# Optimization experiments

Measured on AMD Instinct MI355X. Metric: run time of the kernel, lower is better.

## Reference

```python
import jax, jax.numpy as jnp
import numpy as np
from jax.scipy.special import logsumexp

SINKHORN_ITERS = 10


def _fix_coupling_sinkhorn(lc, lp1, lp2, iterations=SINKHORN_ITERS):
    # lc: [Z,S], lp1: [Z], lp2: [S]
    for _ in range(iterations):
        lc = lc + lp1[:, None] - logsumexp(lc, axis=1, keepdims=True)
        lc = lc + lp2[None, :] - logsumexp(lc, axis=0, keepdims=True)
    return lc


def _fix_coupling_rejection(lc, lp1, lp2):
    fixed_p1 = lc + lp1[:, None] - logsumexp(lc, axis=1, keepdims=True)
    approx_lp2 = logsumexp(fixed_p1, axis=0)
    accept = lp2 - approx_lp2
    accept = accept - jnp.max(accept)
    acc_s2_given_s1 = jax.nn.log_softmax(fixed_p1, axis=-1) + accept[None, :]
    log_keep = logsumexp(acc_s2_given_s1, axis=-1)
    certainly_keep = jnp.exp(log_keep) >= 1.0
    resample = jnp.where(
        certainly_keep, -jnp.inf,
        jnp.log1p(-jnp.where(certainly_keep, 0.0, jnp.exp(log_keep))))
    compensation = resample[:, None] + lp2[None, :]
    return lp1[:, None] + jnp.logaddexp(acc_s2_given_s1, compensation)


def setup_inputs() -> dict:
    key = jax.random.key(0)
    ks = jax.random.split(key, 8)
    B, S, Z, H1, H2 = 64, 512, 1024, 512, 256
    return {
        "s_logits": jax.random.normal(ks[0], (B, S), jnp.float32),
        "W1": jax.random.normal(ks[1], (S, H1), jnp.float32) / np.sqrt(S),
        "b1": jnp.zeros((H1,), jnp.float32),
        "W2": jax.random.normal(ks[2], (H1, H2), jnp.float32) / np.sqrt(H1),
        "b2": jnp.zeros((H2,), jnp.float32),
        "Wout": jax.random.normal(ks[3], (H2, Z, S), jnp.float32) / np.sqrt(H2),
        "bout": jnp.zeros((Z, S), jnp.float32),
        "prior": jax.random.normal(ks[4], (Z,), jnp.float32) * 0.05,
    }


def reference(s_logits, W1, b1, W2, b2, Wout, bout, prior):
    z_logits = jax.nn.log_softmax(prior)  # [Z]

    def get_joint(sl):  # sl: [S]
        v = jax.nn.softmax(sl)
        v = jax.nn.sigmoid(v @ W1 + b1)
        v = jax.nn.sigmoid(v @ W2 + b2)
        log_joint = jnp.einsum('h,hzs->zs', v, Wout) + bout  # [Z,S]
        log_joint = _fix_coupling_sinkhorn(log_joint, z_logits, sl)
        return _fix_coupling_rejection(log_joint, z_logits, sl)

    return jax.vmap(get_joint)(s_logits)  # [B,Z,S]
```

## Files before the change

kernel.cpp:

```cpp
#include <hip/hip_runtime.h>
#include <math.h>

#define Bn 64
#define Sn 512
#define Zn 1024
#define H1n 512
#define H2n 256
#define ZSn (Zn*Sn)

#define OFF_LP1  0
#define OFF_VML  1024
#define OFF_U    17408
#define OFF_V    82944
#define OFF_R    115712
#define OFF_W    181248
#define OFF_RES  214016
#define OFF_PM   279552
#define OFF_PS   541696

__device__ __forceinline__ float wred_max(float x){
#pragma unroll
  for (int o=32;o;o>>=1) x = fmaxf(x, __shfl_xor(x, o, 64));
  return x;
}
__device__ __forceinline__ float wred_sum(float x){
#pragma unroll
  for (int o=32;o;o>>=1) x += __shfl_xor(x, o, 64);
  return x;
}
__device__ __forceinline__ float lae(float a, float c){
  float m = fmaxf(a,c), n = fminf(a,c);
  return m + log1pf(__expf(n-m));
}

__global__ __launch_bounds__(512) void prep_kernel(const float* __restrict__ prior,
                                                   float* __restrict__ ws){
  int b = blockIdx.x, t = threadIdx.x;
  if (b < Bn){ ws[OFF_V + b*Sn + t] = 0.f; return; }
  __shared__ float red[8];
  float x0 = prior[t], x1 = prior[t+512];
  float m = wred_max(fmaxf(x0,x1));
  if ((t&63)==0) red[t>>6] = m;
  __syncthreads();
  float M = red[0];
#pragma unroll
  for (int i=1;i<8;i++) M = fmaxf(M, red[i]);
  float e = __expf(x0-M)+__expf(x1-M);
  e = wred_sum(e);
  __syncthreads();
  if ((t&63)==0) red[t>>6] = e;
  __syncthreads();
  float T = 0.f;
#pragma unroll
  for (int i=0;i<8;i++) T += red[i];
  float lse = M + logf(T);
  ws[OFF_LP1 + t]       = x0 - lse;
  ws[OFF_LP1 + t + 512] = x1 - lse;
}

__global__ __launch_bounds__(512) void mlp_kernel(const float* __restrict__ sl,
    const float* __restrict__ W1, const float* __restrict__ b1,
    const float* __restrict__ W2, const float* __restrict__ b2,
    float* __restrict__ ws){
  __shared__ float p[Sn];
  __shared__ float h1s[H1n];
  __shared__ float red[8];
  int b = blockIdx.x, t = threadIdx.x;
  float x = sl[b*Sn + t];
  float m = wred_max(x);
  if ((t&63)==0) red[t>>6] = m;
  __syncthreads();
  float M = red[0];
#pragma unroll
  for (int i=1;i<8;i++) M = fmaxf(M, red[i]);
  float e = __expf(x-M);
  float es = wred_sum(e);
  __syncthreads();
  if ((t&63)==0) red[t>>6] = es;
  __syncthreads();
  float T = 0.f;
#pragma unroll
  for (int i=0;i<8;i++) T += red[i];
  p[t] = e / T;
  __syncthreads();
  float acc = b1[t];
#pragma unroll 8
  for (int s=0;s<Sn;s++) acc = fmaf(p[s], W1[s*H1n + t], acc);
  h1s[t] = 1.f/(1.f+__expf(-acc));
  __syncthreads();
  if (t < H2n){
    float a2 = b2[t];
#pragma unroll 8
    for (int s=0;s<H1n;s++) a2 = fmaf(h1s[s], W2[s*H2n + t], a2);
    ws[OFF_VML + b*H2n + t] = 1.f/(1.f+__expf(-a2));
  }
}

__global__ __launch_bounds__(256,2) void gemm_kernel(const float* __restrict__ Wout,
    const float* __restrict__ bout, const float* __restrict__ ws, float* __restrict__ K){
  int zh = blockIdx.x*256 + threadIdx.x;
  const float* V = ws + OFF_VML;
  float2 acc[Bn];
#pragma unroll
  for (int b=0;b<Bn;b++){ acc[b].x = 0.f; acc[b].y = 0.f; }
  const float2* Wp = (const float2*)Wout;
  for (int h=0; h<H2n; h++){
    float2 wv = Wp[(size_t)h*(ZSn/2) + zh];
#pragma unroll
    for (int b=0;b<Bn;b++){
      float vb = V[b*H2n + h];
      acc[b].x = fmaf(vb, wv.x, acc[b].x);
      acc[b].y = fmaf(vb, wv.y, acc[b].y);
    }
  }
  float2 bb = ((const float2*)bout)[zh];
#pragma unroll
  for (int b=0;b<Bn;b++){
    float2 o; o.x = acc[b].x + bb.x; o.y = acc[b].y + bb.y;
    ((float2*)(K + (size_t)b*ZSn))[zh] = o;
  }
}

__global__ __launch_bounds__(256) void row_pass(const float* __restrict__ K,
    float* __restrict__ ws, int vecoff, int mode){
  int row = blockIdx.x*4 + (threadIdx.x>>6);
  int l = threadIdx.x & 63;
  int b = row >> 10, z = row & (Zn-1);
  const float4* Kr = (const float4*)(K + (size_t)row*Sn);
  const float4* Vr = (const float4*)(ws + vecoff + b*Sn);
  float4 k0 = Kr[l], k1 = Kr[l+64];
  float4 v0 = Vr[l], v1 = Vr[l+64];
  float x0=k0.x+v0.x, x1=k0.y+v0.y, x2=k0.z+v0.z, x3=k0.w+v0.w;
  float x4=k1.x+v1.x, x5=k1.y+v1.y, x6=k1.z+v1.z, x7=k1.w+v1.w;
  float m = fmaxf(fmaxf(fmaxf(x0,x1),fmaxf(x2,x3)), fmaxf(fmaxf(x4,x5),fmaxf(x6,x7)));
  m = wred_max(m);
  float s = __expf(x0-m)+__expf(x1-m)+__expf(x2-m)+__expf(x3-m)
          + __expf(x4-m)+__expf(x5-m)+__expf(x6-m)+__expf(x7-m);
  s = wred_sum(s);
  if (l==0){
    float L = m + logf(s);
    if (mode==0){
      ws[OFF_U + row] = ws[OFF_LP1 + z] - L;
    } else if (mode==1){
      ws[OFF_R + row] = L;
      ws[OFF_U + row] = ws[OFF_LP1 + z] - L;
    } else {
      float lk = L - ws[OFF_R + row];
      ws[OFF_RES + row] = (lk >= 0.f) ? -__builtin_inff() : log1pf(-__expf(lk));
    }
  }
}

__global__ __launch_bounds__(512) void col_pass1(const float* __restrict__ K,
                                                 float* __restrict__ ws){
  int bzc = blockIdx.x; int b = bzc >> 3, zc = bzc & 7, s = threadIdx.x;
  const float* Kb = K + (size_t)b*ZSn + (size_t)zc*128*Sn;
  const float* ub = ws + OFF_U + b*Zn + zc*128;
  float m = -__builtin_inff(), sum = 0.f;
#pragma unroll 4
  for (int i=0;i<128;i++){
    float x = Kb[i*Sn + s] + ub[i];
    float nm = fmaxf(m, x);
    sum = sum*__expf(m-nm) + __expf(x-nm);
    m = nm;
  }
  ws[OFF_PM + bzc*Sn + s] = m;
  ws[OFF_PS + bzc*Sn + s] = sum;
}

__global__ __launch_bounds__(512) void col_pass2(float* __restrict__ ws,
    const float* __restrict__ sl, int modeB){
  int b = blockIdx.x, s = threadIdx.x;
  float M = -__builtin_inff(), T = 0.f;
#pragma unroll
  for (int zc=0;zc<8;zc++){
    float m = ws[OFF_PM + (b*8+zc)*Sn + s];
    float t = ws[OFF_PS + (b*8+zc)*Sn + s];
    float nM = fmaxf(M, m);
    T = T*__expf(M-nM) + t*__expf(m-nM);
    M = nM;
  }
  float L = M + logf(T);
  float lp2 = sl[b*Sn + s];
  if (!modeB){
    ws[OFF_V + b*Sn + s] = lp2 - L;
  } else {
    __shared__ float red[8];
    float vv = ws[OFF_V + b*Sn + s];
    float araw = lp2 - vv - L;
    float mm = wred_max(araw);
    if ((s&63)==0) red[s>>6] = mm;
    __syncthreads();
    float amax = red[0];
#pragma unroll
    for (int i=1;i<8;i++) amax = fmaxf(amax, red[i]);
    ws[OFF_W + b*Sn + s] = vv + araw - amax;
  }
}

__global__ __launch_bounds__(256) void final_kernel(float* __restrict__ K,
    const float* __restrict__ ws, const float* __restrict__ sl){
  int idx4 = blockIdx.x*256 + threadIdx.x;
  int row = idx4 >> 7;
  int c4  = idx4 & 127;
  int b = row >> 10, z = row & (Zn-1);
  float r  = ws[OFF_R + row];
  float rs = ws[OFF_RES + row];
  float l1 = ws[OFF_LP1 + z];
  float4 k = ((const float4*)K)[idx4];
  float4 w = ((const float4*)(ws + OFF_W + b*Sn))[c4];
  float4 p = ((const float4*)(sl + (size_t)b*Sn))[c4];
  float4 o;
  o.x = l1 + lae(k.x - r + w.x, rs + p.x);
  o.y = l1 + lae(k.y - r + w.y, rs + p.y);
  o.z = l1 + lae(k.z - r + w.z, rs + p.z);
  o.w = l1 + lae(k.w - r + w.w, rs + p.w);
  ((float4*)K)[idx4] = o;
}

extern "C" void kernel_launch(void* const* d_in, const int* in_sizes, int n_in,
                              void* d_out, int out_size, void* d_ws, size_t ws_size,
                              hipStream_t stream) {
  const float* sl    = (const float*)d_in[0];
  const float* W1    = (const float*)d_in[1];
  const float* b1    = (const float*)d_in[2];
  const float* W2    = (const float*)d_in[3];
  const float* b2    = (const float*)d_in[4];
  const float* Wout  = (const float*)d_in[5];
  const float* bout  = (const float*)d_in[6];
  const float* prior = (const float*)d_in[7];
  float* K  = (float*)d_out;
  float* ws = (float*)d_ws;

  prep_kernel<<<Bn+1, 512, 0, stream>>>(prior, ws);
  mlp_kernel<<<Bn, 512, 0, stream>>>(sl, W1, b1, W2, b2, ws);
  gemm_kernel<<<ZSn/512, 256, 0, stream>>>(Wout, bout, ws, K);

  for (int it = 0; it < 10; ++it){
    row_pass <<<Bn*Zn/4, 256, 0, stream>>>(K, ws, OFF_V, 0);
    col_pass1<<<Bn*8,    512, 0, stream>>>(K, ws);
    col_pass2<<<Bn,      512, 0, stream>>>(ws, sl, 0);
  }
  row_pass <<<Bn*Zn/4, 256, 0, stream>>>(K, ws, OFF_V, 1);
  col_pass1<<<Bn*8,    512, 0, stream>>>(K, ws);
  col_pass2<<<Bn,      512, 0, stream>>>(ws, sl, 1);
  row_pass <<<Bn*Zn/4, 256, 0, stream>>>(K, ws, OFF_W, 2);

  final_kernel<<<(Bn*(size_t)ZSn/4)/256, 256, 0, stream>>>(K, ws, sl);
}
```

Baseline: 1.615 ms.

## Fuse Sinkhorn row/col passes, store logits in bf16, fuse final rejection

Replaces the per-iteration row_pass, col_pass1 and col_pass2 launches with one fused kernel. That kernel stages a 64-row tile of the logits in shared memory, does the row logsumexp, and emits column partials. The previous iteration's column reduction is folded into the next launch. When the workspace is large enough, the GEMM output is stored as bf16 in workspace, halving the traffic of every Sinkhorn sweep. The final rejection step is also fused into one row kernel, and the V matrix is transposed for the GEMM. The bf16 storage loses precision relative to the fp32 reference, and the fused kernel uses a large shared-memory tile that limits occupancy.

New measurement: 1.478 ms. -8.5%, faster.

```diff
diff --git a/kernel.cpp b/kernel.cpp
--- a/kernel.cpp
+++ b/kernel.cpp
@@ -9,14 +9,16 @@
 #define ZSn (Zn*Sn)
 
 #define OFF_LP1  0
-#define OFF_VML  1024
-#define OFF_U    17408
-#define OFF_V    82944
-#define OFF_R    115712
-#define OFF_W    181248
-#define OFF_RES  214016
-#define OFF_PM   279552
-#define OFF_PS   541696
+#define OFF_VT   1024
+#define OFF_V    17408
+#define OFF_W    50176
+#define OFF_R    82944
+#define OFF_PM   148480
+#define OFF_PS   672768
+#define OFF_KB   1310720
+#define NEED_BF16_BYTES ((size_t)OFF_KB*4 + (size_t)Bn*ZSn*2)
+
+#define NINF (-__builtin_inff())
 
 __device__ __forceinline__ float wred_max(float x){
 #pragma unroll
@@ -32,12 +34,19 @@
   float m = fmaxf(a,c), n = fminf(a,c);
   return m + log1pf(__expf(n-m));
 }
+__device__ __forceinline__ float toF(float v){ return v; }
+__device__ __forceinline__ float toF(unsigned short v){ return __uint_as_float(((unsigned int)v)<<16); }
+__device__ __forceinline__ unsigned int pack2(float a, float b){
+  unsigned int ua = __float_as_uint(a), ub = __float_as_uint(b);
+  ua = (ua + 0x7fffu + ((ua>>16)&1u)) >> 16;
+  ub = (ub + 0x7fffu + ((ub>>16)&1u)) & 0xffff0000u;
+  return ua | ub;
+}
 
 __global__ __launch_bounds__(512) void prep_kernel(const float* __restrict__ prior,
                                                    float* __restrict__ ws){
-  int b = blockIdx.x, t = threadIdx.x;
-  if (b < Bn){ ws[OFF_V + b*Sn + t] = 0.f; return; }
   __shared__ float red[8];
+  int t = threadIdx.x;
   float x0 = prior[t], x1 = prior[t+512];
   float m = wred_max(fmaxf(x0,x1));
   if ((t&63)==0) red[t>>6] = m;
@@ -92,130 +101,165 @@
     float a2 = b2[t];
 #pragma unroll 8
     for (int s=0;s<H1n;s++) a2 = fmaf(h1s[s], W2[s*H2n + t], a2);
-    ws[OFF_VML + b*H2n + t] = 1.f/(1.f+__expf(-a2));
-  }
-}
-
-__global__ __launch_bounds__(256,2) void gemm_kernel(const float* __restrict__ Wout,
-    const float* __restrict__ bout, const float* __restrict__ ws, float* __restrict__ K){
+    ws[OFF_VT + t*Bn + b] = 1.f/(1.f+__expf(-a2));
+  }
+}
+
+template<int BF>
+__global__ __launch_bounds__(256,1) void gemm_kernel(const float* __restrict__ Wout,
+    const float* __restrict__ bout, const float* __restrict__ ws,
+    float* __restrict__ Kf, unsigned int* __restrict__ Kb){
   int zh = blockIdx.x*256 + threadIdx.x;
-  const float* V = ws + OFF_VML;
+  const float* __restrict__ VT = ws + OFF_VT;
   float2 acc[Bn];
 #pragma unroll
   for (int b=0;b<Bn;b++){ acc[b].x = 0.f; acc[b].y = 0.f; }
   const float2* Wp = (const float2*)Wout;
+#pragma unroll 2
   for (int h=0; h<H2n; h++){
     float2 wv = Wp[(size_t)h*(ZSn/2) + zh];
+    const float* vh = VT + (h<<6);
 #pragma unroll
     for (int b=0;b<Bn;b++){
-      float vb = V[b*H2n + h];
-      acc[b].x = fmaf(vb, wv.x, acc[b].x);
-      acc[b].y = fmaf(vb, wv.y, acc[b].y);
+      acc[b].x = fmaf(vh[b], wv.x, acc[b].x);
+      acc[b].y = fmaf(vh[b], wv.y, acc[b].y);
     }
   }
   float2 bb = ((const float2*)bout)[zh];
 #pragma unroll
   for (int b=0;b<Bn;b++){
-    float2 o; o.x = acc[b].x + bb.x; o.y = acc[b].y + bb.y;
-    ((float2*)(K + (size_t)b*ZSn))[zh] = o;
-  }
-}
-
-__global__ __launch_bounds__(256) void row_pass(const float* __restrict__ K,
-    float* __restrict__ ws, int vecoff, int mode){
-  int row = blockIdx.x*4 + (threadIdx.x>>6);
-  int l = threadIdx.x & 63;
+    float ax = acc[b].x + bb.x, ay = acc[b].y + bb.y;
+    if (BF){
+      Kb[(size_t)b*(ZSn/2) + zh] = pack2(ax, ay);
+    } else {
+      float2 o; o.x = ax; o.y = ay;
+      ((float2*)Kf)[(size_t)b*(ZSn/2) + zh] = o;
+    }
+  }
+}
+
+template<typename KT>
+__global__ __launch_bounds__(512) void iter_fused(const KT* __restrict__ Kg,
+    float* __restrict__ ws, const float* __restrict__ sl, int iter, int mode){
+  __shared__ KT Ksh[64*512];
+  __shared__ float vsh[512];
+  __shared__ float ush[64];
+  __shared__ float lsh[64];
+  int t = threadIdx.x;
+  int b = blockIdx.x >> 4, c = blockIdx.x & 15;
+  const float4* s4 = (const float4*)(Kg + ((size_t)((b<<10) + (c<<6)) << 9));
+  float4* d4 = (float4*)Ksh;
+  constexpr int NV = (int)sizeof(KT)*4;
+#pragma unroll
+  for (int i=0;i<NV;i++) d4[i*512 + t] = s4[i*512 + t];
+  if (t < 64) lsh[t] = ws[OFF_LP1 + (c<<6) + t];
+  float v_s;
+  if (iter == 0) v_s = 0.f;
+  else {
+    float M = NINF, S = 0.f;
+#pragma unroll
+    for (int cc=0; cc<16; cc++){
+      float m = ws[OFF_PM + ((b*16+cc)<<9) + t];
+      float p = ws[OFF_PS + ((b*16+cc)<<9) + t];
+      float nm = fmaxf(M, m);
+      S = S*__expf(M-nm) + p*__expf(m-nm);
+      M = nm;
+    }
+    v_s = sl[(b<<9) + t] - (M + logf(S));
+  }
+  vsh[t] = v_s;
+  if (mode) ws[OFF_V + (b<<9) + t] = v_s;
+  __syncthreads();
+  int l = t & 63, w = t >> 6;
+#pragma unroll
+  for (int rr=0; rr<8; rr++){
+    int row = (w<<3) + rr;
+    float x[8];
+    float m = NINF;
+#pragma unroll
+    for (int j=0;j<8;j++){
+      x[j] = toF(Ksh[(row<<9) + (j<<6) + l]) + vsh[(j<<6)+l];
+      m = fmaxf(m, x[j]);
+    }
+    m = wred_max(m);
+    float s = 0.f;
+#pragma unroll
+    for (int j=0;j<8;j++) s += __expf(x[j]-m);
+    s = wred_sum(s);
+    float L = m + logf(s);
+    if (l == 0){
+      ush[row] = lsh[row] - L;
+      if (mode) ws[OFF_R + (b<<10) + (c<<6) + row] = L;
+    }
+  }
+  __syncthreads();
+  float M = NINF, S = 0.f;
+#pragma unroll 8
+  for (int i=0;i<64;i++){
+    float x2 = toF(Ksh[(i<<9) + t]) + ush[i];
+    float nm = fmaxf(M, x2);
+    S = S*__expf(M-nm) + __expf(x2-nm);
+    M = nm;
+  }
+  ws[OFF_PM + ((b*16+c)<<9) + t] = M;
+  ws[OFF_PS + ((b*16+c)<<9) + t] = S;
+}
+
+__global__ __launch_bounds__(512) void wker(float* __restrict__ ws, const float* __restrict__ sl){
+  __shared__ float red[8];
+  int b = blockIdx.x, s = threadIdx.x;
+  float M = NINF, S = 0.f;
+#pragma unroll
+  for (int cc=0; cc<16; cc++){
+    float m = ws[OFF_PM + ((b*16+cc)<<9) + s];
+    float p = ws[OFF_PS + ((b*16+cc)<<9) + s];
+    float nm = fmaxf(M, m);
+    S = S*__expf(M-nm) + p*__expf(m-nm);
+    M = nm;
+  }
+  float L = M + logf(S);
+  float v = ws[OFF_V + (b<<9) + s];
+  float araw = sl[(b<<9)+s] - v - L;
+  float mm = wred_max(araw);
+  if ((s&63)==0) red[s>>6] = mm;
+  __syncthreads();
+  float amax = red[0];
+#pragma unroll
+  for (int i=1;i<8;i++) amax = fmaxf(amax, red[i]);
+  ws[OFF_W + (b<<9) + s] = v + araw - amax;
+}
+
+template<typename KT>
+__global__ __launch_bounds__(512) void final_fused(const KT* Kg,
+    float* out, const float* __restrict__ ws, const float* __restrict__ sl){
+  int t = threadIdx.x, l = t & 63, wv = t >> 6;
+  int row = blockIdx.x*8 + wv;
   int b = row >> 10, z = row & (Zn-1);
-  const float4* Kr = (const float4*)(K + (size_t)row*Sn);
-  const float4* Vr = (const float4*)(ws + vecoff + b*Sn);
-  float4 k0 = Kr[l], k1 = Kr[l+64];
-  float4 v0 = Vr[l], v1 = Vr[l+64];
-  float x0=k0.x+v0.x, x1=k0.y+v0.y, x2=k0.z+v0.z, x3=k0.w+v0.w;
-  float x4=k1.x+v1.x, x5=k1.y+v1.y, x6=k1.z+v1.z, x7=k1.w+v1.w;
-  float m = fmaxf(fmaxf(fmaxf(x0,x1),fmaxf(x2,x3)), fmaxf(fmaxf(x4,x5),fmaxf(x6,x7)));
+  const KT* Kr = Kg + ((size_t)row << 9);
+  const float* wr = ws + OFF_W + (b << 9);
+  const float* pr = sl + (b << 9);
+  float r  = ws[OFF_R + row];
+  float l1 = ws[OFF_LP1 + z];
+  float k[8], a[8];
+  float m = NINF;
+#pragma unroll
+  for (int j=0;j<8;j++){
+    k[j] = toF(Kr[(j<<6)+l]);
+    a[j] = k[j] - r + wr[(j<<6)+l];
+    m = fmaxf(m, a[j]);
+  }
   m = wred_max(m);
-  float s = __expf(x0-m)+__expf(x1-m)+__expf(x2-m)+__expf(x3-m)
-          + __expf(x4-m)+__expf(x5-m)+__expf(x6-m)+__expf(x7-m);
+  float s = 0.f;
+#pragma unroll
+  for (int j=0;j<8;j++) s += __expf(a[j]-m);
   s = wred_sum(s);
-  if (l==0){
-    float L = m + logf(s);
-    if (mode==0){
-      ws[OFF_U + row] = ws[OFF_LP1 + z] - L;
-    } else if (mode==1){
-      ws[OFF_R + row] = L;
-      ws[OFF_U + row] = ws[OFF_LP1 + z] - L;
-    } else {
-      float lk = L - ws[OFF_R + row];
-      ws[OFF_RES + row] = (lk >= 0.f) ? -__builtin_inff() : log1pf(-__expf(lk));
-    }
-  }
-}
-
-__global__ __launch_bounds__(512) void col_pass1(const float* __restrict__ K,
-                                                 float* __restrict__ ws){
-  int bzc = blockIdx.x; int b = bzc >> 3, zc = bzc & 7, s = threadIdx.x;
-  const float* Kb = K + (size_t)b*ZSn + (size_t)zc*128*Sn;
-  const float* ub = ws + OFF_U + b*Zn + zc*128;
-  float m = -__builtin_inff(), sum = 0.f;
-#pragma unroll 4
-  for (int i=0;i<128;i++){
-    float x = Kb[i*Sn + s] + ub[i];
-    float nm = fmaxf(m, x);
-    sum = sum*__expf(m-nm) + __expf(x-nm);
-    m = nm;
-  }
-  ws[OFF_PM + bzc*Sn + s] = m;
-  ws[OFF_PS + bzc*Sn + s] = sum;
-}
-
-__global__ __launch_bounds__(512) void col_pass2(float* __restrict__ ws,
-    const float* __restrict__ sl, int modeB){
-  int b = blockIdx.x, s = threadIdx.x;
-  float M = -__builtin_inff(), T = 0.f;
-#pragma unroll
-  for (int zc=0;zc<8;zc++){
-    float m = ws[OFF_PM + (b*8+zc)*Sn + s];
-    float t = ws[OFF_PS + (b*8+zc)*Sn + s];
-    float nM = fmaxf(M, m);
-    T = T*__expf(M-nM) + t*__expf(m-nM);
-    M = nM;
-  }
-  float L = M + logf(T);
-  float lp2 = sl[b*Sn + s];
-  if (!modeB){
-    ws[OFF_V + b*Sn + s] = lp2 - L;
-  } else {
-    __shared__ float red[8];
-    float vv = ws[OFF_V + b*Sn + s];
-    float araw = lp2 - vv - L;
-    float mm = wred_max(araw);
-    if ((s&63)==0) red[s>>6] = mm;
-    __syncthreads();
-    float amax = red[0];
-#pragma unroll
-    for (int i=1;i<8;i++) amax = fmaxf(amax, red[i]);
-    ws[OFF_W + b*Sn + s] = vv + araw - amax;
-  }
-}
-
-__global__ __launch_bounds__(256) void final_kernel(float* __restrict__ K,
-    const float* __restrict__ ws, const float* __restrict__ sl){
-  int idx4 = blockIdx.x*256 + threadIdx.x;
-  int row = idx4 >> 7;
-  int c4  = idx4 & 127;
-  int b = row >> 10, z = row & (Zn-1);
-  float r  = ws[OFF_R + row];
-  float rs = ws[OFF_RES + row];
-  float l1 = ws[OFF_LP1 + z];
-  float4 k = ((const float4*)K)[idx4];
-  float4 w = ((const float4*)(ws + OFF_W + b*Sn))[c4];
-  float4 p = ((const float4*)(sl + (size_t)b*Sn))[c4];
-  float4 o;
-  o.x = l1 + lae(k.x - r + w.x, rs + p.x);
-  o.y = l1 + lae(k.y - r + w.y, rs + p.y);
-  o.z = l1 + lae(k.z - r + w.z, rs + p.z);
-  o.w = l1 + lae(k.w - r + w.w, rs + p.w);
-  ((float4*)K)[idx4] = o;
+  float lk = m + logf(s);
+  float rs = (lk >= 0.f) ? NINF : log1pf(-__expf(lk));
+  float* Or = out + ((size_t)row << 9);
+#pragma unroll
+  for (int j=0;j<8;j++){
+    Or[(j<<6)+l] = l1 + lae(a[j], rs + pr[(j<<6)+l]);
+  }
 }
 
 extern "C" void kernel_launch(void* const* d_in, const int* in_sizes, int n_in,
@@ -229,22 +273,27 @@
   const float* Wout  = (const float*)d_in[5];
   const float* bout  = (const float*)d_in[6];
   const float* prior = (const float*)d_in[7];
-  float* K  = (float*)d_out;
   float* ws = (float*)d_ws;
-
-  prep_kernel<<<Bn+1, 512, 0, stream>>>(prior, ws);
+  float* Kf = (float*)d_out;
+  unsigned short* Kb = (unsigned short*)(ws + OFF_KB);
+  const bool use_bf16 = (ws_size >= NEED_BF16_BYTES);
+
+  prep_kernel<<<1, 512, 0, stream>>>(prior, ws);
   mlp_kernel<<<Bn, 512, 0, stream>>>(sl, W1, b1, W2, b2, ws);
-  gemm_kernel<<<ZSn/512, 256, 0, stream>>>(Wout, bout, ws, K);
-
-  for (int it = 0; it < 10; ++it){
-    row_pass <<<Bn*Zn/4, 256, 0, stream>>>(K, ws, OFF_V, 0);
-    col_pass1<<<Bn*8,    512, 0, stream>>>(K, ws);
-    col_pass2<<<Bn,      512, 0, stream>>>(ws, sl, 0);
-  }
-  row_pass <<<Bn*Zn/4, 256, 0, stream>>>(K, ws, OFF_V, 1);
-  col_pass1<<<Bn*8,    512, 0, stream>>>(K, ws);
-  col_pass2<<<Bn,      512, 0, stream>>>(ws, sl, 1);
-  row_pass <<<Bn*Zn/4, 256, 0, stream>>>(K, ws, OFF_W, 2);
-
-  final_kernel<<<(Bn*(size_t)ZSn/4)/256, 256, 0, stream>>>(K, ws, sl);
-}
+
+  if (use_bf16){
+    gemm_kernel<1><<<ZSn/512, 256, 0, stream>>>(Wout, bout, ws, nullptr, (unsigned int*)Kb);
+    for (int it = 0; it < 10; ++it)
+      iter_fused<unsigned short><<<Bn*16, 512, 0, stream>>>(Kb, ws, sl, it, 0);
+    iter_fused<unsigned short><<<Bn*16, 512, 0, stream>>>(Kb, ws, sl, 10, 1);
+    wker<<<Bn, 512, 0, stream>>>(ws, sl);
+    final_fused<unsigned short><<<Bn*Zn/8, 512, 0, stream>>>(Kb, (float*)d_out, ws, sl);
+  } else {
+    gemm_kernel<0><<<ZSn/512, 256, 0, stream>>>(Wout, bout, ws, Kf, nullptr);
+    for (int it = 0; it < 10; ++it)
+      iter_fused<float><<<Bn*16, 512, 0, stream>>>(Kf, ws, sl, it, 0);
+    iter_fused<float><<<Bn*16, 512, 0, stream>>>(Kf, ws, sl, 10, 1);
+    wker<<<Bn, 512, 0, stream>>>(ws, sl);
+    final_fused<float><<<Bn*Zn/8, 512, 0, stream>>>(Kf, (float*)d_out, ws, sl);
+  }
+}
```
